# Performance work log

Hardware: AMD Instinct MI355X
Metric: run time of the kernel (lower is better)

## Reference

```python
import jax, jax.numpy as jnp
import numpy as np

VOCAB = 21128
D_WENLAN = 2048
SENT_LEN = 44  # hard-coded in original forward


def setup_inputs() -> dict:
    key = jax.random.key(0)
    ks = jax.random.split(key, 8)
    B, S, P = 32, 8, 32
    L = S * SENT_LEN  # 352
    concat_output = jax.random.normal(ks[0], (B, S, D_WENLAN), jnp.float32)
    input_ids = jax.random.randint(ks[1], (B, L), 0, VOCAB, jnp.int32)
    topic_ids = jax.random.randint(ks[2], (B, P), 0, VOCAB, jnp.int32)
    tpw_att_mask = jnp.ones((B, P), jnp.int32)
    tpw_type_ids = jnp.zeros((B, P), jnp.int32)
    attention_mask = jnp.ones((B, L), jnp.int32)
    type_ids = jax.random.randint(ks[3], (B, L), 0, 8, jnp.int32)
    token_table = jax.random.normal(ks[4], (VOCAB, D_WENLAN), jnp.float32) * 0.02
    W1 = jax.random.normal(ks[5], (D_WENLAN, 512), jnp.float32) * 0.02
    b1 = jnp.zeros((512,), jnp.float32)
    W2 = jax.random.normal(ks[6], (512, 768), jnp.float32) * 0.02
    b2 = jnp.zeros((768,), jnp.float32)
    return dict(concat_output=concat_output, input_ids=input_ids, topic_ids=topic_ids,
                tpw_att_mask=tpw_att_mask, tpw_type_ids=tpw_type_ids,
                attention_mask=attention_mask, type_ids=type_ids,
                token_table=token_table, W1=W1, b1=b1, W2=W2, b2=b2)


def reference(concat_output, input_ids, topic_ids, tpw_att_mask, tpw_type_ids,
              attention_mask, type_ids, token_table, W1, b1, W2, b2):
    B, S, D = concat_output.shape
    # vectorized replacement of the python double-loop dict lookups:
    topic_emb = token_table[topic_ids]                      # [B,P,2048]
    inp_emb = token_table[input_ids]                        # [B,L,2048]
    # scatter-add: each sentence block of 44 tokens gets its concat_output row added
    inp_emb = inp_emb.reshape(B, S, SENT_LEN, D) + concat_output[:, :, None, :]
    input_embs = jnp.concatenate([topic_emb, inp_emb.reshape(B, S * SENT_LEN, D)], axis=1)
    # projector MLP (Linear -> tanh -> Linear)
    h = jnp.tanh(jnp.einsum('btd,dk->btk', input_embs, W1) + b1)
    gpt_input_embs = jnp.einsum('btk,ke->bte', h, W2) + b2   # [B,P+L,768]
    # auxiliary concatenated tensors fed to gpt2 (is_train=True path)
    labels = jnp.concatenate([topic_ids, input_ids], axis=1)
    full_type_ids = jnp.concatenate([tpw_type_ids, type_ids], axis=1)
    full_att_mask = jnp.concatenate([tpw_att_mask, attention_mask], axis=1)
    return gpt_input_embs, labels, full_type_ids, full_att_mask
```

## Files before the change

kernel.cpp:

```cpp
#include <hip/hip_runtime.h>
#include <math.h>

typedef _Float16 half8 __attribute__((ext_vector_type(8)));
typedef float f32x4 __attribute__((ext_vector_type(4)));

#define BB 32
#define SS 8
#define PP 32
#define SENT 44
#define LL 352
#define TT 384
#define DD 2048
#define H1 512
#define H2 768
#define MM (BB*TT)
#define OUT0 (MM*H2)

#define GLL16(g, l) __builtin_amdgcn_global_load_lds( \
    (const __attribute__((address_space(1))) void*)(g), \
    (__attribute__((address_space(3))) void*)(l), 16, 0, 0)

__global__ __launch_bounds__(256) void gather_kernel(
    const float* __restrict__ token_table,
    const int*   __restrict__ topic_ids,
    const int*   __restrict__ input_ids,
    const float* __restrict__ concat_output,
    const int*   __restrict__ tpw_type_ids,
    const int*   __restrict__ type_ids,
    const int*   __restrict__ tpw_att_mask,
    const int*   __restrict__ attention_mask,
    _Float16*    __restrict__ A16,
    float*       __restrict__ out)
{
    const int m = blockIdx.x;
    const int b = m / TT;
    const int t = m % TT;
    const float* src;
    const float* addp = nullptr;
    int tok;
    if (t < PP) {
        tok = topic_ids[b * PP + t];
        src = token_table + (size_t)tok * DD;
    } else {
        int u = t - PP;
        tok = input_ids[b * LL + u];
        src = token_table + (size_t)tok * DD;
        addp = concat_output + ((size_t)b * SS + (u / SENT)) * DD;
    }
    if (threadIdx.x == 0) {
        int ty, mk;
        if (t < PP) {
            ty = tpw_type_ids[b * PP + t];
            mk = tpw_att_mask[b * PP + t];
        } else {
            int u = t - PP;
            ty = type_ids[b * LL + u];
            mk = attention_mask[b * LL + u];
        }
        out[OUT0 + m]          = (float)tok;
        out[OUT0 + MM + m]     = (float)ty;
        out[OUT0 + 2 * MM + m] = (float)mk;
    }
    _Float16* dst = A16 + (size_t)m * DD;
    const int base = threadIdx.x * 8;
    float4 v0 = *(const float4*)(src + base);
    float4 v1 = *(const float4*)(src + base + 4);
    if (addp) {
        float4 c0 = *(const float4*)(addp + base);
        float4 c1 = *(const float4*)(addp + base + 4);
        v0.x += c0.x; v0.y += c0.y; v0.z += c0.z; v0.w += c0.w;
        v1.x += c1.x; v1.y += c1.y; v1.z += c1.z; v1.w += c1.w;
    }
    half8 h;
    h[0] = (_Float16)v0.x; h[1] = (_Float16)v0.y; h[2] = (_Float16)v0.z; h[3] = (_Float16)v0.w;
    h[4] = (_Float16)v1.x; h[5] = (_Float16)v1.y; h[6] = (_Float16)v1.z; h[7] = (_Float16)v1.w;
    *(half8*)(dst + base) = h;
}

__global__ __launch_bounds__(256) void transpose_f16_kernel(
    const float* __restrict__ src, _Float16* __restrict__ dst, int R, int C)
{
    __shared__ float tile[32][33];
    int c0 = blockIdx.x * 32;
    int r0 = blockIdx.y * 32;
    int tx = threadIdx.x & 31;
    int ty = threadIdx.x >> 5;
    #pragma unroll
    for (int i = 0; i < 4; ++i)
        tile[ty + i*8][tx] = src[(size_t)(r0 + ty + i*8) * C + c0 + tx];
    __syncthreads();
    #pragma unroll
    for (int i = 0; i < 4; ++i)
        dst[(size_t)(c0 + ty + i*8) * R + r0 + tx] = (_Float16)tile[tx][ty + i*8];
}

__global__ __launch_bounds__(256) void gemm1_kernel(
    const _Float16* __restrict__ A16,
    const _Float16* __restrict__ W1T,
    const float*    __restrict__ b1,
    _Float16*       __restrict__ Hout)
{
    const int tid  = threadIdx.x;
    const int wid  = tid >> 6;
    const int lane = tid & 63;

    const int logical = ((blockIdx.x & 7) * 192) + (blockIdx.x >> 3);
    const int bm = logical >> 3;
    const int bn = logical & 7;

    __shared__ _Float16 As[3][64 * 32];
    __shared__ _Float16 Bs[3][64 * 32];

    const int rl = lane >> 2;
    const int cg = lane & 3;
    const _Float16* asrc = A16 + (size_t)(bm * 64 + wid * 16 + rl) * DD
                               + (cg << 3);
    const _Float16* bsrc = W1T + (size_t)(bn * 64 + wid * 16 + rl) * DD
                               + (cg << 3);

    #define G1_ISSUE(slot, k0) {                                           \
        GLL16(asrc + (k0), &As[slot][(wid * 16) * 32]);                    \
        GLL16(bsrc + (k0), &Bs[slot][(wid * 16) * 32]);                    \
    }

    const int wrow = (wid >> 1) * 32;
    const int wcol = (wid & 1) * 32;
    const int fr   = lane & 15;
    const int fg   = lane >> 4;

    f32x4 acc[2][2] = {};

    const int NT = DD / 32;

    G1_ISSUE(0, 0);
    G1_ISSUE(1, 32);

    int cs = 0;
    for (int t = 0; t < NT; ++t) {
        if (t + 2 < NT) {
            const int is = (cs + 2 >= 3) ? cs - 1 : cs + 2;
            G1_ISSUE(is, (t + 2) * 32);
            asm volatile("s_waitcnt vmcnt(4)" ::: "memory");
        } else if (t + 1 < NT) {
            asm volatile("s_waitcnt vmcnt(2)" ::: "memory");
        } else {
            asm volatile("s_waitcnt vmcnt(0)" ::: "memory");
        }
        __builtin_amdgcn_s_barrier();
        __builtin_amdgcn_s_setprio(1);
        {
            half8 af[2], bf[2];
            #pragma unroll
            for (int i = 0; i < 2; ++i)
                af[i] = *(const half8*)&As[cs][(wrow + i * 16 + fr) * 32 + fg * 8];
            #pragma unroll
            for (int j = 0; j < 2; ++j)
                bf[j] = *(const half8*)&Bs[cs][(wcol + j * 16 + fr) * 32 + fg * 8];
            #pragma unroll
            for (int i = 0; i < 2; ++i)
                #pragma unroll
                for (int j = 0; j < 2; ++j)
                    acc[i][j] = __builtin_amdgcn_mfma_f32_16x16x32_f16(
                        af[i], bf[j], acc[i][j], 0, 0, 0);
        }
        __builtin_amdgcn_s_setprio(0);
        __builtin_amdgcn_s_barrier();
        cs = (cs + 1 >= 3) ? 0 : cs + 1;
    }

    #pragma unroll
    for (int i = 0; i < 2; ++i) {
        #pragma unroll
        for (int j = 0; j < 2; ++j) {
            int col = bn * 64 + wcol + j * 16 + fr;
            float bias = b1[col];
            #pragma unroll
            for (int r = 0; r < 4; ++r) {
                int row = bm * 64 + wrow + i * 16 + fg * 4 + r;
                Hout[(size_t)row * H1 + col] = (_Float16)tanhf(acc[i][j][r] + bias);
            }
        }
    }
    #undef G1_ISSUE
}

__global__ __launch_bounds__(256) void gemm2_kernel(
    const _Float16* __restrict__ Hin,
    const _Float16* __restrict__ W2T,
    const float*    __restrict__ b2,
    float*          __restrict__ out)
{
    const int tid  = threadIdx.x;
    const int wid  = tid >> 6;
    const int lane = tid & 63;

    const int logical = ((blockIdx.x & 7) * 64) + (blockIdx.x >> 3);
    const int bm = logical >> 2;
    const int bn = logical & 3;

    __shared__ _Float16 As[2][96 * 64];
    __shared__ _Float16 Bs[2][192 * 64];

    const int rl = lane >> 3;
    const int cg = lane & 7;
    const _Float16* asrc = Hin + (size_t)(bm * 96 + wid * 24 + rl) * H1
                               + ((cg ^ rl) << 3);
    const _Float16* bsrc = W2T + (size_t)(bn * 192 + wid * 48 + rl) * H1
                               + ((cg ^ rl) << 3);

    #define G2_ISSUE(buf, k0) {                                           \
        _Pragma("unroll")                                                 \
        for (int q = 0; q < 3; ++q)                                       \
            GLL16(asrc + (size_t)q * 8 * H1 + (k0),                       \
                  &As[buf][(wid * 3 + q) * 512]);                         \
        _Pragma("unroll")                                                 \
        for (int q = 0; q < 6; ++q)                                       \
            GLL16(bsrc + (size_t)q * 8 * H1 + (k0),                       \
                  &Bs[buf][(wid * 6 + q) * 512]);                         \
    }

    const int wrow = (wid >> 1) * 48;
    const int wcol = (wid & 1) * 96;
    const int fr   = lane & 15;
    const int fg   = lane >> 4;

    f32x4 acc[3][6] = {};

    G2_ISSUE(0, 0);

    const int NT = H1 / 64;
    for (int t = 0; t < NT; ++t) {
        __syncthreads();
        if (t + 1 < NT) G2_ISSUE((t + 1) & 1, (t + 1) * 64);
        const int cb = t & 1;
        #pragma unroll
        for (int kk = 0; kk < 2; ++kk) {
            half8 af[3], bf[6];
            #pragma unroll
            for (int i = 0; i < 3; ++i) {
                int row = wrow + i * 16 + fr;
                af[i] = *(const half8*)&As[cb][
                    (row * 64 + kk * 32 + fg * 8) ^ ((row & 7) << 3)];
            }
            #pragma unroll
            for (int j = 0; j < 6; ++j) {
                int row = wcol + j * 16 + fr;
                bf[j] = *(const half8*)&Bs[cb][
                    (row * 64 + kk * 32 + fg * 8) ^ ((row & 7) << 3)];
            }
            #pragma unroll
            for (int i = 0; i < 3; ++i)
                #pragma unroll
                for (int j = 0; j < 6; ++j)
                    acc[i][j] = __builtin_amdgcn_mfma_f32_16x16x32_f16(af[i], bf[j], acc[i][j], 0, 0, 0);
        }
    }

    #pragma unroll
    for (int i = 0; i < 3; ++i) {
        #pragma unroll
        for (int j = 0; j < 6; ++j) {
            int col = bn * 192 + wcol + j * 16 + fr;
            float bias = b2[col];
            #pragma unroll
            for (int r = 0; r < 4; ++r) {
                int row = bm * 96 + wrow + i * 16 + fg * 4 + r;
                out[(size_t)row * H2 + col] = acc[i][j][r] + bias;
            }
        }
    }
    #undef G2_ISSUE
}

extern "C" void kernel_launch(void* const* d_in, const int* in_sizes, int n_in,
                              void* d_out, int out_size, void* d_ws, size_t ws_size,
                              hipStream_t stream) {
    const float* concat_output  = (const float*)d_in[0];
    const int*   input_ids      = (const int*)d_in[1];
    const int*   topic_ids      = (const int*)d_in[2];
    const int*   tpw_att_mask   = (const int*)d_in[3];
    const int*   tpw_type_ids   = (const int*)d_in[4];
    const int*   attention_mask = (const int*)d_in[5];
    const int*   type_ids       = (const int*)d_in[6];
    const float* token_table    = (const float*)d_in[7];
    const float* W1             = (const float*)d_in[8];
    const float* b1             = (const float*)d_in[9];
    const float* W2             = (const float*)d_in[10];
    const float* b2             = (const float*)d_in[11];
    float* out = (float*)d_out;

    _Float16* w1t = (_Float16*)d_ws;
    _Float16* w2t = w1t + (size_t)H1 * DD;
    _Float16* Hws = w2t + (size_t)H2 * H1;
    _Float16* A16 = Hws + (size_t)MM * H1;

    transpose_f16_kernel<<<dim3(H1 / 32, DD / 32), 256, 0, stream>>>(W1, w1t, DD, H1);
    transpose_f16_kernel<<<dim3(H2 / 32, H1 / 32), 256, 0, stream>>>(W2, w2t, H1, H2);
    gather_kernel<<<MM, 256, 0, stream>>>(
        token_table, topic_ids, input_ids, concat_output,
        tpw_type_ids, type_ids, tpw_att_mask, attention_mask, A16, out);

    gemm1_kernel<<<(MM / 64) * (H1 / 64), 256, 0, stream>>>(A16, w1t, b1, Hws);
    gemm2_kernel<<<(MM / 96) * (H2 / 192), 256, 0, stream>>>(Hws, w2t, b2, out);
}
```

Baseline: 106.0 us.

## Use single-wave blocks for gemm1 and drop workgroup barriers

gemm1 now launches 64-thread blocks in which one wave computes the whole 64x64 tile with a 4x4 MFMA accumulator grid, in place of four waves each computing a 32x32 quadrant. Each wave issues all the async global-to-LDS loads for its own tile, so the per-iteration s_barrier pairs and setprio calls can go, and the vmcnt waits are scaled to match. The aim is to remove workgroup synchronisation overhead and give each wave more MFMA work per LDS fragment load. In exchange each wave holds more registers, and per-CU occupancy and memory-level parallelism now depend on many small blocks being resident at once.

```diff
diff --git a/kernel.cpp b/kernel.cpp
--- a/kernel.cpp
+++ b/kernel.cpp
@@ -94,15 +94,13 @@
         dst[(size_t)(c0 + ty + i*8) * R + r0 + tx] = (_Float16)tile[tx][ty + i*8];
 }
 
-__global__ __launch_bounds__(256) void gemm1_kernel(
+__global__ __launch_bounds__(64) void gemm1_kernel(
     const _Float16* __restrict__ A16,
     const _Float16* __restrict__ W1T,
     const float*    __restrict__ b1,
     _Float16*       __restrict__ Hout)
 {
-    const int tid  = threadIdx.x;
-    const int wid  = tid >> 6;
-    const int lane = tid & 63;
+    const int lane = threadIdx.x;
 
     const int logical = ((blockIdx.x & 7) * 192) + (blockIdx.x >> 3);
     const int bm = logical >> 3;
@@ -113,22 +111,23 @@
 
     const int rl = lane >> 2;
     const int cg = lane & 3;
-    const _Float16* asrc = A16 + (size_t)(bm * 64 + wid * 16 + rl) * DD
-                               + (cg << 3);
-    const _Float16* bsrc = W1T + (size_t)(bn * 64 + wid * 16 + rl) * DD
-                               + (cg << 3);
-
-    #define G1_ISSUE(slot, k0) {                                           \
-        GLL16(asrc + (k0), &As[slot][(wid * 16) * 32]);                    \
-        GLL16(bsrc + (k0), &Bs[slot][(wid * 16) * 32]);                    \
-    }
-
-    const int wrow = (wid >> 1) * 32;
-    const int wcol = (wid & 1) * 32;
-    const int fr   = lane & 15;
-    const int fg   = lane >> 4;
-
-    f32x4 acc[2][2] = {};
+    const _Float16* asrc = A16 + (size_t)(bm * 64 + rl) * DD + (cg << 3);
+    const _Float16* bsrc = W1T + (size_t)(bn * 64 + rl) * DD + (cg << 3);
+
+    #define G1_ISSUE(slot, k0) {                                            \
+        _Pragma("unroll")                                                   \
+        for (int q = 0; q < 4; ++q) {                                       \
+            GLL16(asrc + (size_t)q * 16 * DD + (k0),                        \
+                  &As[slot][(q * 16) * 32]);                                \
+            GLL16(bsrc + (size_t)q * 16 * DD + (k0),                        \
+                  &Bs[slot][(q * 16) * 32]);                                \
+        }                                                                   \
+    }
+
+    const int fr = lane & 15;
+    const int fg = lane >> 4;
+
+    f32x4 acc[4][4] = {};
 
     const int NT = DD / 32;
 
@@ -140,43 +139,40 @@
         if (t + 2 < NT) {
             const int is = (cs + 2 >= 3) ? cs - 1 : cs + 2;
             G1_ISSUE(is, (t + 2) * 32);
-            asm volatile("s_waitcnt vmcnt(4)" ::: "memory");
+            asm volatile("s_waitcnt vmcnt(16)" ::: "memory");
         } else if (t + 1 < NT) {
-            asm volatile("s_waitcnt vmcnt(2)" ::: "memory");
+            asm volatile("s_waitcnt vmcnt(8)" ::: "memory");
         } else {
             asm volatile("s_waitcnt vmcnt(0)" ::: "memory");
         }
-        __builtin_amdgcn_s_barrier();
-        __builtin_amdgcn_s_setprio(1);
+        __builtin_amdgcn_sched_barrier(0);
         {
-            half8 af[2], bf[2];
-            #pragma unroll
-            for (int i = 0; i < 2; ++i)
-                af[i] = *(const half8*)&As[cs][(wrow + i * 16 + fr) * 32 + fg * 8];
-            #pragma unroll
-            for (int j = 0; j < 2; ++j)
-                bf[j] = *(const half8*)&Bs[cs][(wcol + j * 16 + fr) * 32 + fg * 8];
-            #pragma unroll
-            for (int i = 0; i < 2; ++i)
+            half8 af[4], bf[4];
+            #pragma unroll
+            for (int i = 0; i < 4; ++i)
+                af[i] = *(const half8*)&As[cs][(i * 16 + fr) * 32 + fg * 8];
+            #pragma unroll
+            for (int j = 0; j < 4; ++j)
+                bf[j] = *(const half8*)&Bs[cs][(j * 16 + fr) * 32 + fg * 8];
+            #pragma unroll
+            for (int i = 0; i < 4; ++i)
                 #pragma unroll
-                for (int j = 0; j < 2; ++j)
+                for (int j = 0; j < 4; ++j)
                     acc[i][j] = __builtin_amdgcn_mfma_f32_16x16x32_f16(
                         af[i], bf[j], acc[i][j], 0, 0, 0);
         }
-        __builtin_amdgcn_s_setprio(0);
-        __builtin_amdgcn_s_barrier();
         cs = (cs + 1 >= 3) ? 0 : cs + 1;
     }
 
     #pragma unroll
-    for (int i = 0; i < 2; ++i) {
+    for (int i = 0; i < 4; ++i) {
         #pragma unroll
-        for (int j = 0; j < 2; ++j) {
-            int col = bn * 64 + wcol + j * 16 + fr;
+        for (int j = 0; j < 4; ++j) {
+            int col = bn * 64 + j * 16 + fr;
             float bias = b1[col];
             #pragma unroll
             for (int r = 0; r < 4; ++r) {
-                int row = bm * 64 + wrow + i * 16 + fg * 4 + r;
+                int row = bm * 64 + i * 16 + fg * 4 + r;
                 Hout[(size_t)row * H1 + col] = (_Float16)tanhf(acc[i][j][r] + bias);
             }
         }
@@ -300,6 +296,6 @@
         token_table, topic_ids, input_ids, concat_output,
         tpw_type_ids, type_ids, tpw_att_mask, attention_mask, A16, out);
 
-    gemm1_kernel<<<(MM / 64) * (H1 / 64), 256, 0, stream>>>(A16, w1t, b1, Hws);
+    gemm1_kernel<<<(MM / 64) * (H1 / 64), 64, 0, stream>>>(A16, w1t, b1, Hws);
     gemm2_kernel<<<(MM / 96) * (H2 / 192), 256, 0, stream>>>(Hws, w2t, b2, out);
 }
```

New measurement: 104.2 us. Within noise of the previous version (-1.7%).
